# Optimization experiments

Hardware: AMD Instinct MI355X
Metric: run time of the kernel (lower is better)

The kernel has to match this reference:

```python
import jax, jax.numpy as jnp
import numpy as np

N_NODES = 100000
N_EDGES = 6400000
MIN_DIST = 5.0


def setup_inputs() -> dict:
    key = jax.random.key(0)
    k1, k2, k3 = jax.random.split(key, 3)
    pos = jax.random.normal(k1, (N_NODES, 2), dtype=jnp.float32)
    vel = jax.random.normal(k2, (N_NODES, 2), dtype=jnp.float32)
    edge_index = jax.random.randint(k3, (2, N_EDGES), 0, N_NODES, dtype=jnp.int64)
    return {"pos": pos, "vel": vel, "edge_index": edge_index}


def reference(pos, vel, edge_index):
    # h = [pos, vel] per node, shape [N, 4]
    h = jnp.concatenate([pos, vel], axis=-1)
    src, dst = edge_index[0], edge_index[1]  # PyG: h_j = h[src], h_i = h[dst]
    h_dif = h[src] - h[dst]                  # [E, 4]
    pos_dif = h_dif[:, :2]                   # [E, 2]
    vel_dif = h_dif[:, 2:]                   # [E, 2]

    norm = jnp.linalg.norm(pos_dif, axis=1)  # [E]
    safe_norm = jnp.where(norm > 0, norm, 1.0)
    # coll = -sigmoid(-10*(|d|-min_dist)) * d/|d|, nan_to_num(0) where |d|==0
    coll = jnp.where(
        (norm > 0)[:, None],
        -jax.nn.sigmoid(-10.0 * (norm - MIN_DIST))[:, None] * pos_dif / safe_norm[:, None],
        0.0,
    )                                        # [E, 2]
    mean_in = pos_dif / 30.0 + vel_dif       # [E, 2]

    n = pos.shape[0]
    add_out = jax.ops.segment_sum(coll, dst, num_segments=n)      # scatter add
    sums = jax.ops.segment_sum(mean_in, dst, num_segments=n)
    counts = jax.ops.segment_sum(jnp.ones((dst.shape[0], 1), pos.dtype), dst, num_segments=n)
    mean_out = sums / jnp.maximum(counts, 1.0)                    # scatter mean

    return add_out * 5.0 + mean_out          # [N, 2] acceleration
```

## Files before the change

### kernel.cpp

```cpp
#include <hip/hip_runtime.h>


#define DC      200
#define NBK     512
#define NSEG    512
#define EPB     12500
#define ORDCAP  14400
#define KMAX    15
#define BLOCK   256
#define BBLOCK  1024
#define FBLOCK  1024

__device__ __forceinline__ void edge_math(float4 hs, float4 hd,
                                          float& cx, float& cy, float& mx, float& my) {
    float px = hs.x - hd.x;
    float py = hs.y - hd.y;
    float vx = hs.z - hd.z;
    float vy = hs.w - hd.w;
    float norm = sqrtf(px * px + py * py);
    cx = 0.0f; cy = 0.0f;
    if (norm > 0.0f) {
        float sig = 1.0f / (1.0f + expf(10.0f * (norm - 5.0f)));
        float scale = -sig / norm;
        cx = scale * px;
        cy = scale * py;
    }
    mx = px * (1.0f / 30.0f) + vx;
    my = py * (1.0f / 30.0f) + vy;
}

__global__ void prep_kernel(const float2* __restrict__ pos2,
                            const float2* __restrict__ vel2,
                            float4* __restrict__ h4, int n) {
    int i = blockIdx.x * blockDim.x + threadIdx.x;
    if (i < n) {
        float2 p = pos2[i];
        float2 v = vel2[i];
        h4[i] = make_float4(p.x, p.y, v.x, v.y);
    }
}

__global__ __launch_bounds__(BBLOCK) void bin_kernel(
        const int* __restrict__ ei, unsigned* __restrict__ binsout,
        int* __restrict__ incl_g, int n_edges) {
    __shared__ int hist[NBK];
    __shared__ int cur[NBK];
    __shared__ int sa[NBK];
    __shared__ int sb[NBK];
    __shared__ unsigned ord[EPB];

    const int tid = threadIdx.x;
    const long long e0 = (long long)blockIdx.x * EPB;
    const int n_my = (int)min((long long)EPB, (long long)n_edges - e0);
    if (n_my <= 0) return;

    const int* __restrict__ srow = ei + e0;
    const int* __restrict__ drow = ei + n_edges + e0;

    for (int i = tid; i < NBK; i += BBLOCK) hist[i] = 0;
    __syncthreads();

    const bool vec = ((e0 & 3) == 0) && ((n_my & 3) == 0) && ((n_edges & 3) == 0);

    if (vec) {
        const int4* d4 = reinterpret_cast<const int4*>(drow);
        int nv = n_my >> 2;
        for (int i = tid; i < nv; i += BBLOCK) {
            int4 dd = d4[i];
            #pragma unroll
            for (int j = 0; j < 4; ++j) {
                unsigned b = (unsigned)(&dd.x)[j] / DC;
                atomicAdd(&hist[b], 1);
            }
        }
    } else {
        for (int i = tid; i < n_my; i += BBLOCK) {
            unsigned b = (unsigned)drow[i] / DC;
            atomicAdd(&hist[b], 1);
        }
    }
    __syncthreads();

    for (int i = tid; i < NBK; i += BBLOCK) sa[i] = hist[i];
    __syncthreads();
    int* ssrc = sa;
    int* sdst = sb;
    for (int off = 1; off < NBK; off <<= 1) {
        for (int i = tid; i < NBK; i += BBLOCK) {
            int v = ssrc[i];
            if (i >= off) v += ssrc[i - off];
            sdst[i] = v;
        }
        __syncthreads();
        int* t = ssrc; ssrc = sdst; sdst = t;
    }
    for (int i = tid; i < NBK; i += BBLOCK) cur[i] = ssrc[i] - hist[i];
    __syncthreads();

    if (vec) {
        const int4* s4 = reinterpret_cast<const int4*>(srow);
        const int4* d4 = reinterpret_cast<const int4*>(drow);
        int nv = n_my >> 2;
        for (int i = tid; i < nv; i += BBLOCK) {
            int4 ss = s4[i];
            int4 dd = d4[i];
            #pragma unroll
            for (int j = 0; j < 4; ++j) {
                int d = (&dd.x)[j];
                unsigned b = (unsigned)d / DC;
                unsigned rel = (unsigned)d - b * DC;
                int p = atomicAdd(&cur[b], 1);
                ord[p] = ((unsigned)(&ss.x)[j] << 8) | rel;
            }
        }
    } else {
        for (int i = tid; i < n_my; i += BBLOCK) {
            int d = drow[i];
            unsigned b = (unsigned)d / DC;
            unsigned rel = (unsigned)d - b * DC;
            int p = atomicAdd(&cur[b], 1);
            ord[p] = ((unsigned)srow[i] << 8) | rel;
        }
    }
    __syncthreads();

    unsigned* __restrict__ bo = binsout + e0;
    for (int i = tid; i < n_my; i += BBLOCK) bo[i] = ord[i];
    int* __restrict__ ig = incl_g + (size_t)blockIdx.x * NBK;
    for (int i = tid; i < NBK; i += BBLOCK) ig[i] = ssrc[i];
}

__global__ void table_kernel(const int* __restrict__ incl_g,
                             unsigned* __restrict__ tab, int nbb) {
    int j = blockIdx.x * blockDim.x + threadIdx.x;
    int b = blockIdx.y;
    if (j >= nbb) return;
    const int* __restrict__ row = incl_g + (size_t)j * NBK;
    int e = row[b];
    int p = (b == 0) ? 0 : row[b - 1];
    unsigned start = (unsigned)j * EPB + (unsigned)p;
    unsigned cnt = (unsigned)min(e - p, 511);
    tab[(size_t)b * nbb + j] = (start << 9) | cnt;
}

__global__ __launch_bounds__(FBLOCK) void fused_kernel(
        const float4* __restrict__ h4, const unsigned* __restrict__ binsout,
        const unsigned* __restrict__ tab, float* __restrict__ out,
        int nbb, int n_nodes) {
    __shared__ unsigned ord2[ORDCAP];
    __shared__ unsigned stab[NSEG];
    __shared__ int spfx[NSEG + 1];
    __shared__ int hist[DC];
    __shared__ int pfx[DC + 1];
    __shared__ int cur[DC];
    __shared__ int wsum[16];
    __shared__ int wbase[16];

    const int tid  = threadIdx.x;
    const int lane = tid & 63;
    const int wv   = tid >> 6;
    const int dc   = blockIdx.x;
    const unsigned* __restrict__ trow = tab + (size_t)dc * nbb;

    for (int j = tid; j < nbb; j += FBLOCK) stab[j] = trow[j];
    for (int i = tid; i < DC; i += FBLOCK) hist[i] = 0;
    __syncthreads();

    const int nw = (nbb + 63) >> 6;
    if (wv < nw) {
        int i = (wv << 6) + lane;
        int v = (i < nbb) ? (int)(stab[i] & 511u) : 0;
        #pragma unroll
        for (int m = 1; m < 64; m <<= 1) {
            int u = __shfl_up(v, m);
            if (lane >= m) v += u;
        }
        spfx[i + 1] = v;
        if (lane == 63) wsum[wv] = v;
    }
    if (tid == 0) spfx[0] = 0;
    __syncthreads();
    if (tid == 0) {
        int run = 0;
        for (int w2 = 0; w2 < nw; ++w2) { wbase[w2] = run; run += wsum[w2]; }
    }
    __syncthreads();
    if (wv < nw && wv > 0) {
        int i = (wv << 6) + lane;
        spfx[i + 1] += wbase[wv];
    }
    __syncthreads();

    int tot = spfx[nbb];
    if (tot > ORDCAP) tot = ORDCAP;
    const int K = (tot + FBLOCK - 1) / FBLOCK;

    unsigned w[KMAX];
    const int i0  = tid * K;
    const int rem = max(0, min(K, tot - i0));
    int j = 0, off = 0;
    unsigned sj = 0; int cj = 0;
    if (rem > 0) {
        int lo = 0, hi = nbb - 1;
        while (lo < hi) {
            int mid = (lo + hi + 1) >> 1;
            if (spfx[mid] <= i0) lo = mid; else hi = mid - 1;
        }
        j = lo;
        off = i0 - spfx[j];
        unsigned tj = stab[j];
        cj = (int)(tj & 511u);
        sj = tj >> 9;
    }
    #pragma unroll
    for (int q = 0; q < KMAX; ++q) {
        if (q < rem) {
            while (off >= cj) {
                ++j;
                unsigned tj = stab[j];
                cj = (int)(tj & 511u);
                sj = tj >> 9;
                off = 0;
            }
            w[q] = binsout[sj + off];
            ++off;
        }
    }
    #pragma unroll
    for (int q = 0; q < KMAX; ++q)
        if (q < rem) atomicAdd(&hist[w[q] & 255u], 1);
    __syncthreads();

    const int nwh = (DC + 63) >> 6;
    if (wv < nwh) {
        int r = (wv << 6) + lane;
        int v = (r < DC) ? hist[r] : 0;
        #pragma unroll
        for (int m = 1; m < 64; m <<= 1) {
            int u = __shfl_up(v, m);
            if (lane >= m) v += u;
        }
        if (r < DC) pfx[r + 1] = v;
        if (lane == 63) wsum[8 + wv] = v;
    }
    if (tid == 0) pfx[0] = 0;
    __syncthreads();
    if (tid == 0) {
        int run = 0;
        for (int w2 = 0; w2 < nwh; ++w2) { wbase[8 + w2] = run; run += wsum[8 + w2]; }
    }
    __syncthreads();
    if (wv < nwh && wv > 0) {
        int r = (wv << 6) + lane;
        if (r < DC) pfx[r + 1] += wbase[8 + wv];
    }
    __syncthreads();
    for (int r = tid; r < DC; r += FBLOCK) cur[r] = min(pfx[r], ORDCAP);
    __syncthreads();

    #pragma unroll
    for (int q = 0; q < KMAX; ++q) {
        if (q < rem) {
            int p = atomicAdd(&cur[w[q] & 255u], 1);
            if (p < ORDCAP) ord2[p] = w[q] >> 8;
        }
    }
    __syncthreads();

    const int grp = tid >> 4;
    const int gl  = tid & 15;
    const int base = dc * DC;
    for (int r = grp; r < DC; r += FBLOCK / 16) {
        int n = base + r;
        if (n < n_nodes) {
            int st = min(pfx[r], ORDCAP), en = min(pfx[r + 1], ORDCAP);
            int cnt = hist[r];
            float4 hd = h4[n];
            float a0 = 0.f, a1 = 0.f, a2 = 0.f, a3 = 0.f;
            for (int k = st + gl; k < en; k += 16) {
                unsigned s = ord2[k];
                float4 hs = h4[s];
                float cx, cy, mx, my;
                edge_math(hs, hd, cx, cy, mx, my);
                a0 += cx; a1 += cy; a2 += mx; a3 += my;
            }
            #pragma unroll
            for (int m = 8; m >= 1; m >>= 1) {
                a0 += __shfl_xor(a0, m);
                a1 += __shfl_xor(a1, m);
                a2 += __shfl_xor(a2, m);
                a3 += __shfl_xor(a3, m);
            }
            if (gl == 0) {
                float inv = 1.0f / fmaxf((float)cnt, 1.0f);
                float2 o;
                o.x = a0 * 5.0f + a2 * inv;
                o.y = a1 * 5.0f + a3 * inv;
                reinterpret_cast<float2*>(out)[n] = o;
            }
        }
    }
}

__global__ void edge_kernel(const float* __restrict__ pos,
                            const float* __restrict__ vel,
                            const int* __restrict__ ei,
                            float* __restrict__ acc,
                            int n_nodes, int n_edges) {
    int e = blockIdx.x * blockDim.x + threadIdx.x;
    if (e >= n_edges) return;
    int s = ei[e];
    int d = ei[n_edges + e];
    const float2* pos2 = reinterpret_cast<const float2*>(pos);
    const float2* vel2 = reinterpret_cast<const float2*>(vel);
    float4 hs = make_float4(pos2[s].x, pos2[s].y, vel2[s].x, vel2[s].y);
    float4 hd = make_float4(pos2[d].x, pos2[d].y, vel2[d].x, vel2[d].y);
    float cx, cy, mx, my;
    edge_math(hs, hd, cx, cy, mx, my);
    atomicAdd(&acc[0 * n_nodes + d], cx);
    atomicAdd(&acc[1 * n_nodes + d], cy);
    atomicAdd(&acc[2 * n_nodes + d], mx);
    atomicAdd(&acc[3 * n_nodes + d], my);
    atomicAdd(&acc[4 * n_nodes + d], 1.0f);
}

__global__ void finalize_kernel(const float* __restrict__ acc,
                                float* __restrict__ out, int n_nodes) {
    int i = blockIdx.x * blockDim.x + threadIdx.x;
    if (i >= n_nodes) return;
    float cx = acc[0 * n_nodes + i];
    float cy = acc[1 * n_nodes + i];
    float mx = acc[2 * n_nodes + i];
    float my = acc[3 * n_nodes + i];
    float cnt = acc[4 * n_nodes + i];
    float inv = 1.0f / fmaxf(cnt, 1.0f);
    float2 o;
    o.x = cx * 5.0f + mx * inv;
    o.y = cy * 5.0f + my * inv;
    reinterpret_cast<float2*>(out)[i] = o;
}

extern "C" void kernel_launch(void* const* d_in, const int* in_sizes, int n_in,
                              void* d_out, int out_size, void* d_ws, size_t ws_size,
                              hipStream_t stream) {
    const float* pos = (const float*)d_in[0];
    const float* vel = (const float*)d_in[1];
    const int*   ei  = (const int*)d_in[2];
    float* out = (float*)d_out;

    int n_nodes = in_sizes[0] / 2;
    int n_edges = in_sizes[2] / 2;

    int ndc = (n_nodes + DC - 1) / DC;
    int nbb = (int)(((long long)n_edges + EPB - 1) / EPB);

    size_t h_off    = 0;
    size_t bo_off   = (h_off + (size_t)n_nodes * 16 + 511) & ~(size_t)511;
    size_t incl_off = (bo_off + (size_t)nbb * EPB * 4 + 511) & ~(size_t)511;
    size_t tab_off  = (incl_off + (size_t)nbb * NBK * 4 + 511) & ~(size_t)511;
    size_t need     = tab_off + (size_t)ndc * nbb * 4;

    bool start_ok = (size_t)nbb * EPB < (1u << 23);

    if (ndc <= NBK && nbb <= NSEG && need <= ws_size && start_ok &&
        (unsigned)n_nodes < (1u << 24)) {
        float4*   h4      = (float4*)((char*)d_ws + h_off);
        unsigned* binsout = (unsigned*)((char*)d_ws + bo_off);
        int*      incl_g  = (int*)((char*)d_ws + incl_off);
        unsigned* tab     = (unsigned*)((char*)d_ws + tab_off);

        int grid_p = (n_nodes + BLOCK - 1) / BLOCK;
        prep_kernel<<<grid_p, BLOCK, 0, stream>>>(
            (const float2*)pos, (const float2*)vel, h4, n_nodes);

        bin_kernel<<<nbb, BBLOCK, 0, stream>>>(ei, binsout, incl_g, n_edges);

        dim3 tg((nbb + BLOCK - 1) / BLOCK, ndc);
        table_kernel<<<tg, BLOCK, 0, stream>>>(incl_g, tab, nbb);

        fused_kernel<<<ndc, FBLOCK, 0, stream>>>(h4, binsout, tab, out,
                                                 nbb, n_nodes);
    } else {
        float* acc = (float*)d_ws;
        hipMemsetAsync(d_ws, 0, (size_t)5 * n_nodes * sizeof(float), stream);
        int grid_e = (n_edges + BLOCK - 1) / BLOCK;
        edge_kernel<<<grid_e, BLOCK, 0, stream>>>(pos, vel, ei, acc, n_nodes, n_edges);
        int grid_n = (n_nodes + BLOCK - 1) / BLOCK;
        finalize_kernel<<<grid_n, BLOCK, 0, stream>>>(acc, out, n_nodes);
    }
}
```

Before: 151.7 us.

## Drop table kernel, write transposed bin offsets, and register-cache edges in binning

The bin kernel now reads each edge once into registers and reuses them for both the histogram and scatter passes. It replaces the multi-barrier Hillis-Steele scan with a wave-shuffle scan and writes inclusive offsets transposed so the fused kernel can build segment starts directly, which removes the separate table kernel launch. The fused kernel uses a strided element assignment with a fixed-depth binary search per element instead of contiguous chunks with a pointer walk. This saves a launch and one pass over the edge list, at the cost of more registers and a per-element search.

```diff
diff --git a/kernel.cpp b/kernel.cpp
--- a/kernel.cpp
+++ b/kernel.cpp
@@ -6,6 +6,7 @@
 #define NSEG    512
 #define EPB     12500
 #define ORDCAP  14400
+#define KB      13
 #define KMAX    15
 #define BLOCK   256
 #define BBLOCK  1024
@@ -42,15 +43,18 @@
 
 __global__ __launch_bounds__(BBLOCK) void bin_kernel(
         const int* __restrict__ ei, unsigned* __restrict__ binsout,
-        int* __restrict__ incl_g, int n_edges) {
+        int* __restrict__ inclT, int n_edges, int nbb) {
     __shared__ int hist[NBK];
     __shared__ int cur[NBK];
-    __shared__ int sa[NBK];
-    __shared__ int sb[NBK];
     __shared__ unsigned ord[EPB];
-
-    const int tid = threadIdx.x;
-    const long long e0 = (long long)blockIdx.x * EPB;
+    __shared__ int wsum[16];
+    __shared__ int wbase[16];
+
+    const int tid  = threadIdx.x;
+    const int lane = tid & 63;
+    const int wv   = tid >> 6;
+    const int bx   = blockIdx.x;
+    const long long e0 = (long long)bx * EPB;
     const int n_my = (int)min((long long)EPB, (long long)n_edges - e0);
     if (n_my <= 0) return;
 
@@ -60,95 +64,70 @@
     for (int i = tid; i < NBK; i += BBLOCK) hist[i] = 0;
     __syncthreads();
 
-    const bool vec = ((e0 & 3) == 0) && ((n_my & 3) == 0) && ((n_edges & 3) == 0);
-
-    if (vec) {
-        const int4* d4 = reinterpret_cast<const int4*>(drow);
-        int nv = n_my >> 2;
-        for (int i = tid; i < nv; i += BBLOCK) {
-            int4 dd = d4[i];
-            #pragma unroll
-            for (int j = 0; j < 4; ++j) {
-                unsigned b = (unsigned)(&dd.x)[j] / DC;
-                atomicAdd(&hist[b], 1);
-            }
-        }
-    } else {
-        for (int i = tid; i < n_my; i += BBLOCK) {
-            unsigned b = (unsigned)drow[i] / DC;
+    int      bq[KB];
+    unsigned wq[KB];
+    #pragma unroll
+    for (int q = 0; q < KB; ++q) {
+        int idx = tid + q * BBLOCK;
+        if (idx < n_my) {
+            int d = drow[idx];
+            int s = srow[idx];
+            int b = (unsigned)d / DC;
+            bq[q] = b;
+            wq[q] = ((unsigned)s << 8) | (unsigned)(d - b * DC);
             atomicAdd(&hist[b], 1);
-        }
-    }
-    __syncthreads();
-
-    for (int i = tid; i < NBK; i += BBLOCK) sa[i] = hist[i];
-    __syncthreads();
-    int* ssrc = sa;
-    int* sdst = sb;
-    for (int off = 1; off < NBK; off <<= 1) {
-        for (int i = tid; i < NBK; i += BBLOCK) {
-            int v = ssrc[i];
-            if (i >= off) v += ssrc[i - off];
-            sdst[i] = v;
-        }
-        __syncthreads();
-        int* t = ssrc; ssrc = sdst; sdst = t;
-    }
-    for (int i = tid; i < NBK; i += BBLOCK) cur[i] = ssrc[i] - hist[i];
-    __syncthreads();
-
-    if (vec) {
-        const int4* s4 = reinterpret_cast<const int4*>(srow);
-        const int4* d4 = reinterpret_cast<const int4*>(drow);
-        int nv = n_my >> 2;
-        for (int i = tid; i < nv; i += BBLOCK) {
-            int4 ss = s4[i];
-            int4 dd = d4[i];
-            #pragma unroll
-            for (int j = 0; j < 4; ++j) {
-                int d = (&dd.x)[j];
-                unsigned b = (unsigned)d / DC;
-                unsigned rel = (unsigned)d - b * DC;
-                int p = atomicAdd(&cur[b], 1);
-                ord[p] = ((unsigned)(&ss.x)[j] << 8) | rel;
-            }
-        }
-    } else {
-        for (int i = tid; i < n_my; i += BBLOCK) {
-            int d = drow[i];
-            unsigned b = (unsigned)d / DC;
-            unsigned rel = (unsigned)d - b * DC;
-            int p = atomicAdd(&cur[b], 1);
-            ord[p] = ((unsigned)srow[i] << 8) | rel;
+        } else {
+            bq[q] = -1;
+        }
+    }
+    __syncthreads();
+
+    const int nw = NBK >> 6;
+    int myinc = 0, myh = 0, myi = 0;
+    if (wv < nw) {
+        myi = (wv << 6) + lane;
+        myh = hist[myi];
+        int v = myh;
+        #pragma unroll
+        for (int m = 1; m < 64; m <<= 1) {
+            int u = __shfl_up(v, m);
+            if (lane >= m) v += u;
+        }
+        myinc = v;
+        if (lane == 63) wsum[wv] = v;
+    }
+    __syncthreads();
+    if (tid == 0) {
+        int run = 0;
+        for (int w = 0; w < nw; ++w) { wbase[w] = run; run += wsum[w]; }
+    }
+    __syncthreads();
+    if (wv < nw) {
+        int inc = myinc + wbase[wv];
+        cur[myi] = inc - myh;
+        inclT[(size_t)myi * nbb + bx] = inc;
+    }
+    __syncthreads();
+
+    #pragma unroll
+    for (int q = 0; q < KB; ++q) {
+        if (bq[q] >= 0) {
+            int p = atomicAdd(&cur[bq[q]], 1);
+            ord[p] = wq[q];
         }
     }
     __syncthreads();
 
     unsigned* __restrict__ bo = binsout + e0;
     for (int i = tid; i < n_my; i += BBLOCK) bo[i] = ord[i];
-    int* __restrict__ ig = incl_g + (size_t)blockIdx.x * NBK;
-    for (int i = tid; i < NBK; i += BBLOCK) ig[i] = ssrc[i];
-}
-
-__global__ void table_kernel(const int* __restrict__ incl_g,
-                             unsigned* __restrict__ tab, int nbb) {
-    int j = blockIdx.x * blockDim.x + threadIdx.x;
-    int b = blockIdx.y;
-    if (j >= nbb) return;
-    const int* __restrict__ row = incl_g + (size_t)j * NBK;
-    int e = row[b];
-    int p = (b == 0) ? 0 : row[b - 1];
-    unsigned start = (unsigned)j * EPB + (unsigned)p;
-    unsigned cnt = (unsigned)min(e - p, 511);
-    tab[(size_t)b * nbb + j] = (start << 9) | cnt;
 }
 
 __global__ __launch_bounds__(FBLOCK) void fused_kernel(
         const float4* __restrict__ h4, const unsigned* __restrict__ binsout,
-        const unsigned* __restrict__ tab, float* __restrict__ out,
+        const int* __restrict__ inclT, float* __restrict__ out,
         int nbb, int n_nodes) {
     __shared__ unsigned ord2[ORDCAP];
-    __shared__ unsigned stab[NSEG];
+    __shared__ unsigned sstart[NSEG];
     __shared__ int spfx[NSEG + 1];
     __shared__ int hist[DC];
     __shared__ int pfx[DC + 1];
@@ -160,109 +139,93 @@
     const int lane = tid & 63;
     const int wv   = tid >> 6;
     const int dc   = blockIdx.x;
-    const unsigned* __restrict__ trow = tab + (size_t)dc * nbb;
-
-    for (int j = tid; j < nbb; j += FBLOCK) stab[j] = trow[j];
+
+    for (int j = tid; j < nbb; j += FBLOCK) {
+        int hi = inclT[(size_t)dc * nbb + j];
+        int lo = (dc > 0) ? inclT[(size_t)(dc - 1) * nbb + j] : 0;
+        sstart[j] = (unsigned)j * EPB + (unsigned)lo;
+        spfx[j + 1] = hi - lo;
+    }
     for (int i = tid; i < DC; i += FBLOCK) hist[i] = 0;
+    if (tid == 0) spfx[0] = 0;
     __syncthreads();
 
     const int nw = (nbb + 63) >> 6;
+    int myv = 0, myj = -1;
     if (wv < nw) {
-        int i = (wv << 6) + lane;
-        int v = (i < nbb) ? (int)(stab[i] & 511u) : 0;
+        myj = (wv << 6) + lane;
+        int v = (myj < nbb) ? spfx[myj + 1] : 0;
         #pragma unroll
         for (int m = 1; m < 64; m <<= 1) {
             int u = __shfl_up(v, m);
             if (lane >= m) v += u;
         }
-        spfx[i + 1] = v;
+        myv = v;
         if (lane == 63) wsum[wv] = v;
     }
-    if (tid == 0) spfx[0] = 0;
     __syncthreads();
     if (tid == 0) {
         int run = 0;
-        for (int w2 = 0; w2 < nw; ++w2) { wbase[w2] = run; run += wsum[w2]; }
-    }
-    __syncthreads();
-    if (wv < nw && wv > 0) {
-        int i = (wv << 6) + lane;
-        spfx[i + 1] += wbase[wv];
-    }
-    __syncthreads();
-
+        for (int w = 0; w < nw; ++w) { wbase[w] = run; run += wsum[w]; }
+    }
+    __syncthreads();
+    if (wv < nw && myj < nbb) spfx[myj + 1] = myv + wbase[wv];
+    __syncthreads();
     int tot = spfx[nbb];
     if (tot > ORDCAP) tot = ORDCAP;
-    const int K = (tot + FBLOCK - 1) / FBLOCK;
-
-    unsigned w[KMAX];
-    const int i0  = tid * K;
-    const int rem = max(0, min(K, tot - i0));
-    int j = 0, off = 0;
-    unsigned sj = 0; int cj = 0;
-    if (rem > 0) {
-        int lo = 0, hi = nbb - 1;
-        while (lo < hi) {
-            int mid = (lo + hi + 1) >> 1;
-            if (spfx[mid] <= i0) lo = mid; else hi = mid - 1;
-        }
-        j = lo;
-        off = i0 - spfx[j];
-        unsigned tj = stab[j];
-        cj = (int)(tj & 511u);
-        sj = tj >> 9;
-    }
+    for (int j = nbb + tid; j < NSEG; j += FBLOCK) spfx[j + 1] = tot;
+    __syncthreads();
+
+    unsigned wq[KMAX];
     #pragma unroll
     for (int q = 0; q < KMAX; ++q) {
-        if (q < rem) {
-            while (off >= cj) {
-                ++j;
-                unsigned tj = stab[j];
-                cj = (int)(tj & 511u);
-                sj = tj >> 9;
-                off = 0;
-            }
-            w[q] = binsout[sj + off];
-            ++off;
-        }
-    }
-    #pragma unroll
-    for (int q = 0; q < KMAX; ++q)
-        if (q < rem) atomicAdd(&hist[w[q] & 255u], 1);
+        int p = tid + q * FBLOCK;
+        if (p < tot) {
+            int lo = 0;
+            #pragma unroll
+            for (int st = NSEG / 2; st >= 1; st >>= 1)
+                if (spfx[lo + st] <= p) lo += st;
+            unsigned w = binsout[sstart[lo] + (unsigned)(p - spfx[lo])];
+            wq[q] = w;
+            atomicAdd(&hist[w & 255u], 1);
+        }
+    }
     __syncthreads();
 
     const int nwh = (DC + 63) >> 6;
+    int mvr = 0, mr = -1, mh = 0;
     if (wv < nwh) {
-        int r = (wv << 6) + lane;
-        int v = (r < DC) ? hist[r] : 0;
+        mr = (wv << 6) + lane;
+        mh = (mr < DC) ? hist[mr] : 0;
+        int v = mh;
         #pragma unroll
         for (int m = 1; m < 64; m <<= 1) {
             int u = __shfl_up(v, m);
             if (lane >= m) v += u;
         }
-        if (r < DC) pfx[r + 1] = v;
+        mvr = v;
         if (lane == 63) wsum[8 + wv] = v;
     }
-    if (tid == 0) pfx[0] = 0;
     __syncthreads();
     if (tid == 0) {
         int run = 0;
-        for (int w2 = 0; w2 < nwh; ++w2) { wbase[8 + w2] = run; run += wsum[8 + w2]; }
-    }
-    __syncthreads();
-    if (wv < nwh && wv > 0) {
-        int r = (wv << 6) + lane;
-        if (r < DC) pfx[r + 1] += wbase[8 + wv];
-    }
-    __syncthreads();
-    for (int r = tid; r < DC; r += FBLOCK) cur[r] = min(pfx[r], ORDCAP);
+        for (int w = 0; w < nwh; ++w) { wbase[8 + w] = run; run += wsum[8 + w]; }
+    }
+    __syncthreads();
+    if (wv < nwh && mr < DC) {
+        int inc = mvr + wbase[8 + wv];
+        pfx[mr + 1] = inc;
+        cur[mr] = inc - mh;
+        if (mr == 0) pfx[0] = 0;
+    }
     __syncthreads();
 
     #pragma unroll
     for (int q = 0; q < KMAX; ++q) {
-        if (q < rem) {
-            int p = atomicAdd(&cur[w[q] & 255u], 1);
-            if (p < ORDCAP) ord2[p] = w[q] >> 8;
+        int p = tid + q * FBLOCK;
+        if (p < tot) {
+            int pp = atomicAdd(&cur[wq[q] & 255u], 1);
+            ord2[pp] = wq[q] >> 8;
         }
     }
     __syncthreads();
@@ -273,8 +236,8 @@
     for (int r = grp; r < DC; r += FBLOCK / 16) {
         int n = base + r;
         if (n < n_nodes) {
-            int st = min(pfx[r], ORDCAP), en = min(pfx[r + 1], ORDCAP);
-            int cnt = hist[r];
+            int st = pfx[r], en = pfx[r + 1];
+            int cnt = en - st;
             float4 hd = h4[n];
             float a0 = 0.f, a1 = 0.f, a2 = 0.f, a3 = 0.f;
             for (int k = st + gl; k < en; k += 16) {
@@ -357,28 +320,22 @@
     size_t h_off    = 0;
     size_t bo_off   = (h_off + (size_t)n_nodes * 16 + 511) & ~(size_t)511;
     size_t incl_off = (bo_off + (size_t)nbb * EPB * 4 + 511) & ~(size_t)511;
-    size_t tab_off  = (incl_off + (size_t)nbb * NBK * 4 + 511) & ~(size_t)511;
-    size_t need     = tab_off + (size_t)ndc * nbb * 4;
-
-    bool start_ok = (size_t)nbb * EPB < (1u << 23);
-
-    if (ndc <= NBK && nbb <= NSEG && need <= ws_size && start_ok &&
+    size_t need     = incl_off + (size_t)NBK * nbb * 4;
+
+    if (ndc <= NBK && nbb <= NSEG && need <= ws_size &&
         (unsigned)n_nodes < (1u << 24)) {
         float4*   h4      = (float4*)((char*)d_ws + h_off);
         unsigned* binsout = (unsigned*)((char*)d_ws + bo_off);
-        int*      incl_g  = (int*)((char*)d_ws + incl_off);
-        unsigned* tab     = (unsigned*)((char*)d_ws + tab_off);
+        int*      inclT   = (int*)((char*)d_ws + incl_off);
 
         int grid_p = (n_nodes + BLOCK - 1) / BLOCK;
         prep_kernel<<<grid_p, BLOCK, 0, stream>>>(
             (const float2*)pos, (const float2*)vel, h4, n_nodes);
 
-        bin_kernel<<<nbb, BBLOCK, 0, stream>>>(ei, binsout, incl_g, n_edges);
-
-        dim3 tg((nbb + BLOCK - 1) / BLOCK, ndc);
-        table_kernel<<<tg, BLOCK, 0, stream>>>(incl_g, tab, nbb);
-
-        fused_kernel<<<ndc, FBLOCK, 0, stream>>>(h4, binsout, tab, out,
+        bin_kernel<<<nbb, BBLOCK, 0, stream>>>(ei, binsout, inclT,
+                                               n_edges, nbb);
+
+        fused_kernel<<<ndc, FBLOCK, 0, stream>>>(h4, binsout, inclT, out,
                                                  nbb, n_nodes);
     } else {
         float* acc = (float*)d_ws;
```

Result: faster. 145.0 us (-4.4%).
